# Kernel tuning notes

Measured on AMD Instinct MI355X. Metric: run time of the kernel, lower is better.

## Reference

```python
import jax, jax.numpy as jnp
import numpy as np

B, F, NUM_LAYERS, T, DEPTH, C = 256, 128, 4, 2048, 6, 100
L = 2 ** DEPTH  # num_leaves = 64

# bit pattern of the oblivious tree: bit d of leaf_idx (MSB-first),
# matching (leaf_idx // (L >> (d+1))) % 2 in the original double loop
_BITS = np.stack([(np.arange(L) // (L >> (d + 1))) % 2 for d in range(DEPTH)])  # [DEPTH, L]


def setup_inputs() -> dict:
    key = jax.random.key(0)
    k = jax.random.split(key, 5)
    x = jax.random.normal(k[0], (B, F), dtype=jnp.float32)
    sel_W = jax.random.normal(k[1], (NUM_LAYERS, T * DEPTH, F), dtype=jnp.float32) * 0.05
    sel_b = jax.random.normal(k[2], (NUM_LAYERS, T * DEPTH), dtype=jnp.float32) * 0.01
    out_W = jax.random.normal(k[3], (C, NUM_LAYERS * T * L), dtype=jnp.float32) * 0.002
    out_b = jax.random.normal(k[4], (C,), dtype=jnp.float32) * 0.01
    return {"x": x, "sel_W": sel_W, "sel_b": sel_b, "out_W": out_W, "out_b": out_b}


def reference(x, sel_W, sel_b, out_W, out_b):
    bits = jnp.asarray(_BITS, dtype=x.dtype)  # [DEPTH, L]
    layer_outputs = []
    for i in range(NUM_LAYERS):
        # feature selector linear -> [B, T, DEPTH] threshold responses
        fv = jax.nn.sigmoid(x @ sel_W[i].T + sel_b[i]).reshape(B, T, DEPTH)
        # leaf probability = prod over depth of (left or right prob per bit)
        leaf = jnp.ones((B, T, L), dtype=x.dtype)
        for d in range(DEPTH):  # fixed small structural loop (depth=6)
            p = fv[:, :, d:d + 1]                     # [B, T, 1] left prob
            bit = bits[d]                             # [L]
            leaf = leaf * (p * (1.0 - bit) + (1.0 - p) * bit)
        layer_outputs.append(leaf.reshape(B, T * L))
    combined = jnp.concatenate(layer_outputs, axis=1)  # [B, NUM_LAYERS*T*L]
    return combined @ out_W.T + out_b
```

## Files before the change

kernel.cpp:

```cpp
#include <hip/hip_runtime.h>

#define BB 256
#define FF 128
#define CC 100
#define KG 512
#define ITPB 16

typedef short bf16x8 __attribute__((ext_vector_type(8)));
typedef float f32x4 __attribute__((ext_vector_type(4)));
typedef _Float16 f16x8 __attribute__((ext_vector_type(8)));

#define LDS_BARRIER() asm volatile("s_waitcnt lgkmcnt(0)\n\ts_barrier" ::: "memory")

static __device__ inline unsigned short f2bf(float f) {
    unsigned u = __float_as_uint(f);
    u += 0x7fffu + ((u >> 16) & 1u);
    return (unsigned short)(u >> 16);
}
static __device__ inline float bf2f(unsigned short h) {
    return __uint_as_float(((unsigned)h) << 16);
}

__global__ __launch_bounds__(256) void fv_kernel(
    const float* __restrict__ x, const float* __restrict__ selW,
    const float* __restrict__ selb, unsigned short* __restrict__ fvout)
{
    __shared__ unsigned short wt[128 * 136];
    __shared__ unsigned short xt[128 * 136];
    __shared__ float sb[128];

    const int tid = threadIdx.x;
    const int m0 = blockIdx.x * 128;
    const int n0 = blockIdx.y * 128;

    #pragma unroll 4
    for (int pass = 0; pass < 16; ++pass) {
        int idx = pass * 256 + tid;
        int r = idx >> 5, f4 = idx & 31;
        float4 v = *((const float4*)(selW + (size_t)(m0 + r) * FF) + f4);
        float4 vx = *((const float4*)(x + (size_t)(n0 + r) * FF) + f4);
        ushort4 h;
        h.x = f2bf(v.x); h.y = f2bf(v.y); h.z = f2bf(v.z); h.w = f2bf(v.w);
        *(ushort4*)(wt + r * 136 + f4 * 4) = h;
        ushort4 hx;
        hx.x = f2bf(vx.x); hx.y = f2bf(vx.y); hx.z = f2bf(vx.z); hx.w = f2bf(vx.w);
        *(ushort4*)(xt + r * 136 + f4 * 4) = hx;
    }
    if (tid < 128) sb[tid] = selb[m0 + tid];
    __syncthreads();

    const int w = tid >> 6, lane = tid & 63;
    const int q = lane >> 4, l15 = lane & 15;
    const int mq = w & 1, nq = w >> 1;

    f32x4 zero4 = {0.f, 0.f, 0.f, 0.f};
    f32x4 acc[4][4];
    #pragma unroll
    for (int i = 0; i < 4; ++i)
        #pragma unroll
        for (int j = 0; j < 4; ++j) acc[i][j] = zero4;

    #pragma unroll
    for (int ch = 0; ch < 4; ++ch) {
        bf16x8 a[4];
        #pragma unroll
        for (int ms = 0; ms < 4; ++ms)
            a[ms] = *(const bf16x8*)(wt + (mq * 64 + ms * 16 + l15) * 136 + ch * 32 + q * 8);
        #pragma unroll
        for (int ns = 0; ns < 4; ++ns) {
            bf16x8 bfr = *(const bf16x8*)(xt + (nq * 64 + ns * 16 + l15) * 136 + ch * 32 + q * 8);
            #pragma unroll
            for (int ms = 0; ms < 4; ++ms)
                acc[ms][ns] = __builtin_amdgcn_mfma_f32_16x16x32_bf16(a[ms], bfr, acc[ms][ns], 0, 0, 0);
        }
    }

    #pragma unroll
    for (int ms = 0; ms < 4; ++ms) {
        int rowl = mq * 64 + ms * 16 + q * 4;
        #pragma unroll
        for (int ns = 0; ns < 4; ++ns) {
            int b = n0 + nq * 64 + ns * 16 + l15;
            #pragma unroll
            for (int reg = 0; reg < 4; ++reg) {
                int row = m0 + rowl + reg;
                float z = acc[ms][ns][reg] + sb[rowl + reg];
                float p = 1.0f / (1.0f + __expf(-z));
                fvout[(size_t)row * 256 + b] = f2bf(p);
            }
        }
    }
}

__global__ __launch_bounds__(256, 2) void main_gemm(
    const unsigned short* __restrict__ fv, const float* __restrict__ outW,
    _Float16* __restrict__ part16)
{
    __shared__ unsigned short leaf[256 * 72];
    __shared__ unsigned short wt[112 * 72];

    const int tid = threadIdx.x;
    const int kg = blockIdx.x;
    const int w = tid >> 6, lane = tid & 63;
    const int q = lane >> 4, l15 = lane & 15;
    const int cc = tid >> 4, f4 = tid & 15;

    f32x4 zero4 = {0.f, 0.f, 0.f, 0.f};
    f32x4 acc[4][7];
    #pragma unroll
    for (int i = 0; i < 4; ++i)
        #pragma unroll
        for (int j = 0; j < 7; ++j) acc[i][j] = zero4;

    float4 wv[2][7];
    unsigned short pv[2][6];
    #pragma unroll
    for (int pb = 0; pb < 2; ++pb) {
        const int it = kg * ITPB + pb;
        #pragma unroll
        for (int pass = 0; pass < 7; ++pass) {
            const int c = pass * 16 + cc;
            float4 v = make_float4(0.f, 0.f, 0.f, 0.f);
            if (c < CC)
                v = *((const float4*)(outW + (size_t)c * 524288 + (size_t)it * 64) + f4);
            wv[pb][pass] = v;
        }
        const unsigned short* fp = fv + (size_t)it * 1536 + tid;
        #pragma unroll
        for (int d = 0; d < 6; ++d) pv[pb][d] = fp[d * 256];
    }

    #pragma unroll 2
    for (int itl = 0; itl < ITPB; ++itl) {
        const int cur = itl & 1;
        LDS_BARRIER();

        #pragma unroll
        for (int pass = 0; pass < 7; ++pass) {
            const int c = pass * 16 + cc;
            ushort4 h;
            h.x = f2bf(wv[cur][pass].x); h.y = f2bf(wv[cur][pass].y);
            h.z = f2bf(wv[cur][pass].z); h.w = f2bf(wv[cur][pass].w);
            *(ushort4*)(wt + c * 72 + f4 * 4) = h;
        }

        {
            float p0 = bf2f(pv[cur][0]), p1 = bf2f(pv[cur][1]), p2 = bf2f(pv[cur][2]);
            float p3 = bf2f(pv[cur][3]), p4 = bf2f(pv[cur][4]), p5 = bf2f(pv[cur][5]);
            float q0 = 1.f - p0, q1 = 1.f - p1, q2 = 1.f - p2;
            float q3 = 1.f - p3, q4 = 1.f - p4, q5 = 1.f - p5;
            float A[4]  = {p0 * p1, p0 * q1, q0 * p1, q0 * q1};
            float B2[4] = {p2 * p3, p2 * q3, q2 * p3, q2 * q3};
            float C2[4] = {p4 * p5, p4 * q5, q4 * p5, q4 * q5};
            float BC[16];
            #pragma unroll
            for (int m = 0; m < 16; ++m) BC[m] = B2[m >> 2] * C2[m & 3];
            unsigned short* row = leaf + tid * 72;
            #pragma unroll
            for (int j = 0; j < 8; ++j) {
                uint4 dw;
                unsigned int* dwp = (unsigned int*)&dw;
                #pragma unroll
                for (int e = 0; e < 4; ++e) {
                    int l0 = j * 8 + 2 * e;
                    float v0 = A[l0 >> 4] * BC[l0 & 15];
                    float v1 = A[(l0 + 1) >> 4] * BC[(l0 + 1) & 15];
                    dwp[e] = (unsigned)f2bf(v0) | ((unsigned)f2bf(v1) << 16);
                }
                *(uint4*)(row + j * 8) = dw;
            }
        }

        {
            const int itn = kg * ITPB + ((itl + 2) & (ITPB - 1));
            #pragma unroll
            for (int pass = 0; pass < 7; ++pass) {
                const int c = pass * 16 + cc;
                if (c < CC)
                    wv[cur][pass] = *((const float4*)(outW + (size_t)c * 524288 + (size_t)itn * 64) + f4);
            }
            const unsigned short* fp = fv + (size_t)itn * 1536 + tid;
            #pragma unroll
            for (int d = 0; d < 6; ++d) pv[cur][d] = fp[d * 256];
        }

        LDS_BARRIER();

        #pragma unroll
        for (int ch = 0; ch < 2; ++ch) {
            bf16x8 a[4];
            #pragma unroll
            for (int ms = 0; ms < 4; ++ms)
                a[ms] = *(const bf16x8*)(leaf + (w * 64 + ms * 16 + l15) * 72 + ch * 32 + q * 8);
            #pragma unroll
            for (int nt = 0; nt < 7; ++nt) {
                bf16x8 bb = *(const bf16x8*)(wt + (nt * 16 + l15) * 72 + ch * 32 + q * 8);
                #pragma unroll
                for (int ms = 0; ms < 4; ++ms)
                    acc[ms][nt] = __builtin_amdgcn_mfma_f32_16x16x32_bf16(a[ms], bb, acc[ms][nt], 0, 0, 0);
            }
        }
    }

    #pragma unroll
    for (int ms = 0; ms < 4; ++ms) {
        const int brow = w * 64 + ms * 16 + q * 4;
        #pragma unroll
        for (int nt = 0; nt < 7; ++nt) {
            const int c = nt * 16 + l15;
            #pragma unroll
            for (int reg = 0; reg < 4; ++reg)
                part16[((size_t)(brow + reg) * KG + kg) * 112 + c] =
                    (_Float16)acc[ms][nt][reg];
        }
    }
}

__global__ __launch_bounds__(256) void reduce_k(
    const _Float16* __restrict__ part16, const float* __restrict__ outb,
    float* __restrict__ out)
{
    __shared__ float red[16 * 112];
    const int b = blockIdx.x;
    const int tid = threadIdx.x;
    const f16x8* slice = (const f16x8*)(part16 + (size_t)b * (KG * 112));

    if (tid < 224) {
        const int c8 = tid % 14;
        const int kgs = tid / 14;
        float s[8];
        #pragma unroll
        for (int j = 0; j < 8; ++j) s[j] = 0.f;
        #pragma unroll 4
        for (int i = 0; i < 32; ++i) {
            f16x8 v = slice[i * 224 + tid];
            #pragma unroll
            for (int j = 0; j < 8; ++j) s[j] += (float)v[j];
        }
        #pragma unroll
        for (int j = 0; j < 8; ++j) red[kgs * 112 + c8 * 8 + j] = s[j];
    }
    __syncthreads();
    if (tid < CC) {
        float r = outb[tid];
        #pragma unroll
        for (int k = 0; k < 16; ++k) r += red[k * 112 + tid];
        out[b * CC + tid] = r;
    }
}

extern "C" void kernel_launch(void* const* d_in, const int* in_sizes, int n_in,
                              void* d_out, int out_size, void* d_ws, size_t ws_size,
                              hipStream_t stream) {
    const float* x    = (const float*)d_in[0];
    const float* selW = (const float*)d_in[1];
    const float* selb = (const float*)d_in[2];
    const float* outW = (const float*)d_in[3];
    const float* outb = (const float*)d_in[4];
    float* out = (float*)d_out;

    unsigned short* fv = (unsigned short*)d_ws;
    _Float16* part16 = (_Float16*)((char*)d_ws + 25165824);

    fv_kernel<<<dim3(384, 2), 256, 0, stream>>>(x, selW, selb, fv);
    main_gemm<<<KG, 256, 0, stream>>>(fv, outW, part16);
    reduce_k<<<BB, 256, 0, stream>>>(part16, outb, out);
}
```

Baseline: 374.9 us.

## Stage out_W via global_load_lds and double the K-split of main GEMM

Loads the fp32 out_W tile directly from global memory into LDS with global_load_lds, then converts it to bf16 B fragments when reading from LDS. This replaces the register prefetch plus the separate bf16 store into a transposed LDS tile. KG doubles to 1024 with half as many iterations per block, which spreads the work over more blocks, and the reduce kernel's loop grows to match. The old two-deep register double-buffer becomes a single stage with a vmcnt(0) wait each iteration. That can expose load latency, and the larger KG doubles the partial-sum traffic the reduce kernel has to read.

```diff
diff --git a/kernel.cpp b/kernel.cpp
--- a/kernel.cpp
+++ b/kernel.cpp
@@ -1,16 +1,18 @@
 #include <hip/hip_runtime.h>
+#include <hip/hip_bf16.h>
 
 #define BB 256
 #define FF 128
 #define CC 100
-#define KG 512
-#define ITPB 16
+#define KG 1024
+#define ITPB 8
 
 typedef short bf16x8 __attribute__((ext_vector_type(8)));
 typedef float f32x4 __attribute__((ext_vector_type(4)));
 typedef _Float16 f16x8 __attribute__((ext_vector_type(8)));
 
 #define LDS_BARRIER() asm volatile("s_waitcnt lgkmcnt(0)\n\ts_barrier" ::: "memory")
+#define WAIT_VM0() asm volatile("s_waitcnt vmcnt(0)" ::: "memory")
 
 static __device__ inline unsigned short f2bf(float f) {
     unsigned u = __float_as_uint(f);
@@ -19,6 +21,16 @@
 }
 static __device__ inline float bf2f(unsigned short h) {
     return __uint_as_float(((unsigned)h) << 16);
+}
+static __device__ inline unsigned pk2(float a, float b) {
+    __hip_bfloat162 h = __float22bfloat162_rn(float2{a, b});
+    union { __hip_bfloat162 h2; unsigned u; } cv; cv.h2 = h;
+    return cv.u;
+}
+static __device__ inline void gl_lds16(const float* g, float* l) {
+    __builtin_amdgcn_global_load_lds(
+        (const __attribute__((address_space(1))) void*)g,
+        (__attribute__((address_space(3))) void*)l, 16, 0, 0);
 }
 
 __global__ __launch_bounds__(256) void fv_kernel(
@@ -96,14 +108,13 @@
     const unsigned short* __restrict__ fv, const float* __restrict__ outW,
     _Float16* __restrict__ part16)
 {
+    __shared__ float stage[7168];
     __shared__ unsigned short leaf[256 * 72];
-    __shared__ unsigned short wt[112 * 72];
 
     const int tid = threadIdx.x;
     const int kg = blockIdx.x;
     const int w = tid >> 6, lane = tid & 63;
     const int q = lane >> 4, l15 = lane & 15;
-    const int cc = tid >> 4, f4 = tid & 15;
 
     f32x4 zero4 = {0.f, 0.f, 0.f, 0.f};
     f32x4 acc[4][7];
@@ -112,41 +123,31 @@
         #pragma unroll
         for (int j = 0; j < 7; ++j) acc[i][j] = zero4;
 
-    float4 wv[2][7];
-    unsigned short pv[2][6];
-    #pragma unroll
-    for (int pb = 0; pb < 2; ++pb) {
-        const int it = kg * ITPB + pb;
-        #pragma unroll
-        for (int pass = 0; pass < 7; ++pass) {
-            const int c = pass * 16 + cc;
-            float4 v = make_float4(0.f, 0.f, 0.f, 0.f);
-            if (c < CC)
-                v = *((const float4*)(outW + (size_t)c * 524288 + (size_t)it * 64) + f4);
-            wv[pb][pass] = v;
-        }
+    int kk4[7], ccl[7];
+    #pragma unroll
+    for (int j = 0; j < 7; ++j) {
+        unsigned s = (unsigned)(w * 7 + j) * 64u + (unsigned)lane;
+        unsigned k4 = s / 112u, c = s % 112u;
+        kk4[j] = (int)k4;
+        ccl[j] = (c < CC) ? (int)c : 0;
+    }
+
+    unsigned short pv[6];
+    {
+        const int it = kg * ITPB;
         const unsigned short* fp = fv + (size_t)it * 1536 + tid;
         #pragma unroll
-        for (int d = 0; d < 6; ++d) pv[pb][d] = fp[d * 256];
-    }
-
-    #pragma unroll 2
+        for (int d = 0; d < 6; ++d) pv[d] = fp[d * 256];
+        #pragma unroll
+        for (int j = 0; j < 7; ++j)
+            gl_lds16(outW + (size_t)ccl[j] * 524288 + (size_t)it * 64 + kk4[j] * 4,
+                     stage + (w * 7 + j) * 256);
+    }
+
     for (int itl = 0; itl < ITPB; ++itl) {
-        const int cur = itl & 1;
-        LDS_BARRIER();
-
-        #pragma unroll
-        for (int pass = 0; pass < 7; ++pass) {
-            const int c = pass * 16 + cc;
-            ushort4 h;
-            h.x = f2bf(wv[cur][pass].x); h.y = f2bf(wv[cur][pass].y);
-            h.z = f2bf(wv[cur][pass].z); h.w = f2bf(wv[cur][pass].w);
-            *(ushort4*)(wt + c * 72 + f4 * 4) = h;
-        }
-
         {
-            float p0 = bf2f(pv[cur][0]), p1 = bf2f(pv[cur][1]), p2 = bf2f(pv[cur][2]);
-            float p3 = bf2f(pv[cur][3]), p4 = bf2f(pv[cur][4]), p5 = bf2f(pv[cur][5]);
+            float p0 = bf2f(pv[0]), p1 = bf2f(pv[1]), p2 = bf2f(pv[2]);
+            float p3 = bf2f(pv[3]), p4 = bf2f(pv[4]), p5 = bf2f(pv[5]);
             float q0 = 1.f - p0, q1 = 1.f - p1, q2 = 1.f - p2;
             float q3 = 1.f - p3, q4 = 1.f - p4, q5 = 1.f - p5;
             float A[4]  = {p0 * p1, p0 * q1, q0 * p1, q0 * q1};
@@ -163,42 +164,55 @@
                 #pragma unroll
                 for (int e = 0; e < 4; ++e) {
                     int l0 = j * 8 + 2 * e;
-                    float v0 = A[l0 >> 4] * BC[l0 & 15];
-                    float v1 = A[(l0 + 1) >> 4] * BC[(l0 + 1) & 15];
-                    dwp[e] = (unsigned)f2bf(v0) | ((unsigned)f2bf(v1) << 16);
+                    dwp[e] = (unsigned)f2bf(A[l0 >> 4] * BC[l0 & 15]) |
+                             ((unsigned)f2bf(A[(l0 + 1) >> 4] * BC[(l0 + 1) & 15]) << 16);
                 }
                 *(uint4*)(row + j * 8) = dw;
             }
         }
 
-        {
-            const int itn = kg * ITPB + ((itl + 2) & (ITPB - 1));
-            #pragma unroll
-            for (int pass = 0; pass < 7; ++pass) {
-                const int c = pass * 16 + cc;
-                if (c < CC)
-                    wv[cur][pass] = *((const float4*)(outW + (size_t)c * 524288 + (size_t)itn * 64) + f4);
+        WAIT_VM0();
+        LDS_BARRIER();
+
+        #pragma unroll
+        for (int ch = 0; ch < 2; ++ch) {
+            const int k4a = ch * 8 + q * 2;
+            bf16x8 bfrag[7];
+            #pragma unroll
+            for (int nt = 0; nt < 7; ++nt) {
+                const int c = nt * 16 + l15;
+                const float* sp = stage + (size_t)(k4a * 112 + c) * 4;
+                f32x4 lo = *(const f32x4*)sp;
+                f32x4 hi = *(const f32x4*)(sp + 448);
+                union { bf16x8 v; unsigned u[4]; } bu;
+                bu.u[0] = pk2(lo[0], lo[1]);
+                bu.u[1] = pk2(lo[2], lo[3]);
+                bu.u[2] = pk2(hi[0], hi[1]);
+                bu.u[3] = pk2(hi[2], hi[3]);
+                bfrag[nt] = bu.v;
             }
-            const unsigned short* fp = fv + (size_t)itn * 1536 + tid;
-            #pragma unroll
-            for (int d = 0; d < 6; ++d) pv[cur][d] = fp[d * 256];
-        }
-
-        LDS_BARRIER();
-
-        #pragma unroll
-        for (int ch = 0; ch < 2; ++ch) {
             bf16x8 a[4];
             #pragma unroll
             for (int ms = 0; ms < 4; ++ms)
                 a[ms] = *(const bf16x8*)(leaf + (w * 64 + ms * 16 + l15) * 72 + ch * 32 + q * 8);
             #pragma unroll
-            for (int nt = 0; nt < 7; ++nt) {
-                bf16x8 bb = *(const bf16x8*)(wt + (nt * 16 + l15) * 72 + ch * 32 + q * 8);
+            for (int nt = 0; nt < 7; ++nt)
                 #pragma unroll
                 for (int ms = 0; ms < 4; ++ms)
-                    acc[ms][nt] = __builtin_amdgcn_mfma_f32_16x16x32_bf16(a[ms], bb, acc[ms][nt], 0, 0, 0);
-            }
+                    acc[ms][nt] = __builtin_amdgcn_mfma_f32_16x16x32_bf16(a[ms], bfrag[nt], acc[ms][nt], 0, 0, 0);
+        }
+
+        LDS_BARRIER();
+
+        if (itl + 1 < ITPB) {
+            const int itn = kg * ITPB + itl + 1;
+            const unsigned short* fp = fv + (size_t)itn * 1536 + tid;
+            #pragma unroll
+            for (int d = 0; d < 6; ++d) pv[d] = fp[d * 256];
+            #pragma unroll
+            for (int j = 0; j < 7; ++j)
+                gl_lds16(outW + (size_t)ccl[j] * 524288 + (size_t)itn * 64 + kk4[j] * 4,
+                         stage + (w * 7 + j) * 256);
         }
     }
 
@@ -232,7 +246,7 @@
         #pragma unroll
         for (int j = 0; j < 8; ++j) s[j] = 0.f;
         #pragma unroll 4
-        for (int i = 0; i < 32; ++i) {
+        for (int i = 0; i < 64; ++i) {
             f16x8 v = slice[i * 224 + tid];
             #pragma unroll
             for (int j = 0; j < 8; ++j) s[j] += (float)v[j];
```

After: 399.8 us. +6.6%, slower.

## Pre-pack out_W into MFMA fragment layout and build leaf fragments in registers

Applied to the files above, without the earlier changes.

Adds a separate kernel that converts out_W to bf16 and stores it in an MFMA-fragment-ordered layout in workspace. main_gemm then loads B fragments straight from global memory instead of staging through LDS. Leaf probabilities are no longer written to LDS; each wave broadcasts the fv values with shuffles and builds its A fragments in registers, which removes both LDS barriers. The cost is an extra pass that reads all of out_W and writes a bf16 copy each call, and main_gemm loses the two-iteration global prefetch of the weights.

```diff
diff --git a/kernel.cpp b/kernel.cpp
--- a/kernel.cpp
+++ b/kernel.cpp
@@ -1,16 +1,17 @@
 #include <hip/hip_runtime.h>
+#include <hip/hip_bf16.h>
 
 #define BB 256
 #define FF 128
 #define CC 100
 #define KG 512
 #define ITPB 16
+#define NIT 8192
+#define WT_IT 7168
 
 typedef short bf16x8 __attribute__((ext_vector_type(8)));
 typedef float f32x4 __attribute__((ext_vector_type(4)));
 typedef _Float16 f16x8 __attribute__((ext_vector_type(8)));
-
-#define LDS_BARRIER() asm volatile("s_waitcnt lgkmcnt(0)\n\ts_barrier" ::: "memory")
 
 static __device__ inline unsigned short f2bf(float f) {
     unsigned u = __float_as_uint(f);
@@ -19,6 +20,11 @@
 }
 static __device__ inline float bf2f(unsigned short h) {
     return __uint_as_float(((unsigned)h) << 16);
+}
+static __device__ inline unsigned pk2(float a, float b) {
+    __hip_bfloat162 h = __float22bfloat162_rn(float2{a, b});
+    union { __hip_bfloat162 h2; unsigned u; } cv; cv.h2 = h;
+    return cv.u;
 }
 
 __global__ __launch_bounds__(256) void fv_kernel(
@@ -92,18 +98,62 @@
     }
 }
 
+__global__ __launch_bounds__(256) void wt_kernel(
+    const float* __restrict__ outW, unsigned short* __restrict__ Wt)
+{
+    __shared__ unsigned short tile[WT_IT];
+    const int tid = threadIdx.x;
+    const int it = blockIdx.x;
+
+    #pragma unroll
+    for (int i = 0; i < 4; ++i) {
+        int s = i * 256 + tid;
+        if (s < 896) *(uint4*)(tile + s * 8) = make_uint4(0, 0, 0, 0);
+    }
+    __syncthreads();
+
+    const int cr = tid >> 4;
+    const int f4 = tid & 15;
+    const int ch4 = (f4 >> 3) * 4 + ((f4 >> 1) & 3);
+    const int j0 = (f4 & 1) * 4;
+
+    float4 v[7];
+    #pragma unroll
+    for (int pass = 0; pass < 7; ++pass) {
+        const int c = pass * 16 + cr;
+        v[pass] = make_float4(0.f, 0.f, 0.f, 0.f);
+        if (c < CC)
+            v[pass] = *((const float4*)(outW + (size_t)c * 524288 + (size_t)it * 64) + f4);
+    }
+    #pragma unroll
+    for (int pass = 0; pass < 7; ++pass) {
+        const int c = pass * 16 + cr;
+        if (c < CC) {
+            unsigned lo = pk2(v[pass].x, v[pass].y);
+            unsigned hi = pk2(v[pass].z, v[pass].w);
+            *(uint2*)(tile + (ch4 * 112 + c) * 8 + j0) = make_uint2(lo, hi);
+        }
+    }
+    __syncthreads();
+
+    uint4* dst = (uint4*)(Wt + (size_t)it * WT_IT);
+    const uint4* src = (const uint4*)tile;
+    #pragma unroll
+    for (int i = 0; i < 4; ++i) {
+        int s = i * 256 + tid;
+        if (s < 896) dst[s] = src[s];
+    }
+}
+
 __global__ __launch_bounds__(256, 2) void main_gemm(
-    const unsigned short* __restrict__ fv, const float* __restrict__ outW,
+    const unsigned short* __restrict__ fv, const unsigned short* __restrict__ Wt,
     _Float16* __restrict__ part16)
 {
-    __shared__ unsigned short leaf[256 * 72];
-    __shared__ unsigned short wt[112 * 72];
-
     const int tid = threadIdx.x;
     const int kg = blockIdx.x;
     const int w = tid >> 6, lane = tid & 63;
     const int q = lane >> 4, l15 = lane & 15;
-    const int cc = tid >> 4, f4 = tid & 15;
+    const int qh = q >> 1, ql = q & 1;
 
     f32x4 zero4 = {0.f, 0.f, 0.f, 0.f};
     f32x4 acc[4][7];
@@ -112,94 +162,74 @@
         #pragma unroll
         for (int j = 0; j < 7; ++j) acc[i][j] = zero4;
 
-    float4 wv[2][7];
-    unsigned short pv[2][6];
-    #pragma unroll
-    for (int pb = 0; pb < 2; ++pb) {
-        const int it = kg * ITPB + pb;
-        #pragma unroll
-        for (int pass = 0; pass < 7; ++pass) {
-            const int c = pass * 16 + cc;
-            float4 v = make_float4(0.f, 0.f, 0.f, 0.f);
-            if (c < CC)
-                v = *((const float4*)(outW + (size_t)c * 524288 + (size_t)it * 64) + f4);
-            wv[pb][pass] = v;
-        }
-        const unsigned short* fp = fv + (size_t)it * 1536 + tid;
-        #pragma unroll
-        for (int d = 0; d < 6; ++d) pv[pb][d] = fp[d * 256];
-    }
-
-    #pragma unroll 2
+    unsigned short pvb[2][6];
+    {
+        const unsigned short* fp = fv + (size_t)(kg * ITPB) * 1536 + tid;
+        #pragma unroll
+        for (int d = 0; d < 6; ++d) pvb[0][d] = fp[d * 256];
+    }
+
     for (int itl = 0; itl < ITPB; ++itl) {
+        const int it = kg * ITPB + itl;
         const int cur = itl & 1;
-        LDS_BARRIER();
-
-        #pragma unroll
-        for (int pass = 0; pass < 7; ++pass) {
-            const int c = pass * 16 + cc;
-            ushort4 h;
-            h.x = f2bf(wv[cur][pass].x); h.y = f2bf(wv[cur][pass].y);
-            h.z = f2bf(wv[cur][pass].z); h.w = f2bf(wv[cur][pass].w);
-            *(ushort4*)(wt + c * 72 + f4 * 4) = h;
-        }
-
-        {
-            float p0 = bf2f(pv[cur][0]), p1 = bf2f(pv[cur][1]), p2 = bf2f(pv[cur][2]);
-            float p3 = bf2f(pv[cur][3]), p4 = bf2f(pv[cur][4]), p5 = bf2f(pv[cur][5]);
-            float q0 = 1.f - p0, q1 = 1.f - p1, q2 = 1.f - p2;
-            float q3 = 1.f - p3, q4 = 1.f - p4, q5 = 1.f - p5;
-            float A[4]  = {p0 * p1, p0 * q1, q0 * p1, q0 * q1};
-            float B2[4] = {p2 * p3, p2 * q3, q2 * p3, q2 * q3};
-            float C2[4] = {p4 * p5, p4 * q5, q4 * p5, q4 * q5};
-            float BC[16];
-            #pragma unroll
-            for (int m = 0; m < 16; ++m) BC[m] = B2[m >> 2] * C2[m & 3];
-            unsigned short* row = leaf + tid * 72;
-            #pragma unroll
-            for (int j = 0; j < 8; ++j) {
-                uint4 dw;
-                unsigned int* dwp = (unsigned int*)&dw;
-                #pragma unroll
-                for (int e = 0; e < 4; ++e) {
-                    int l0 = j * 8 + 2 * e;
-                    float v0 = A[l0 >> 4] * BC[l0 & 15];
-                    float v1 = A[(l0 + 1) >> 4] * BC[(l0 + 1) & 15];
-                    dwp[e] = (unsigned)f2bf(v0) | ((unsigned)f2bf(v1) << 16);
-                }
-                *(uint4*)(row + j * 8) = dw;
+
+        if (itl + 1 < ITPB) {
+            const unsigned short* fp = fv + (size_t)(it + 1) * 1536 + tid;
+            #pragma unroll
+            for (int d = 0; d < 6; ++d) pvb[cur ^ 1][d] = fp[d * 256];
+        }
+
+        const unsigned short* wbase = Wt + (size_t)it * WT_IT;
+        bf16x8 bfr[2][7];
+        #pragma unroll
+        for (int ch = 0; ch < 2; ++ch)
+            #pragma unroll
+            for (int nt = 0; nt < 7; ++nt)
+                bfr[ch][nt] = *(const bf16x8*)(wbase + ((ch * 4 + q) * 112 + nt * 16 + l15) * 8);
+
+        float p[6];
+        #pragma unroll
+        for (int d = 0; d < 6; ++d) p[d] = bf2f(pvb[cur][d]);
+
+        bf16x8 afr[4][2];
+        #pragma unroll
+        for (int ms = 0; ms < 4; ++ms) {
+            const int src = ms * 16 + l15;
+            float s0 = __shfl(p[0], src, 64);
+            float s1 = __shfl(p[1], src, 64);
+            float s2 = __shfl(p[2], src, 64);
+            float s3 = __shfl(p[3], src, 64);
+            float s4 = __shfl(p[4], src, 64);
+            float s5 = __shfl(p[5], src, 64);
+            float t1 = qh ? (1.f - s1) : s1;
+            float A0 = s0 * t1;
+            float A1 = (1.f - s0) * t1;
+            float t2 = ql ? (1.f - s2) : s2;
+            float Bv0 = t2 * s3;
+            float Bv1 = t2 * (1.f - s3);
+            float n4 = 1.f - s4, n5 = 1.f - s5;
+            float Cv0 = s4 * s5, Cv1 = s4 * n5, Cv2 = n4 * s5, Cv3 = n4 * n5;
+            #pragma unroll
+            for (int ch = 0; ch < 2; ++ch) {
+                float A = ch ? A1 : A0;
+                float ab0 = A * Bv0, ab1 = A * Bv1;
+                union { bf16x8 v; unsigned u[4]; } bu;
+                bu.u[0] = pk2(ab0 * Cv0, ab0 * Cv1);
+                bu.u[1] = pk2(ab0 * Cv2, ab0 * Cv3);
+                bu.u[2] = pk2(ab1 * Cv0, ab1 * Cv1);
+                bu.u[3] = pk2(ab1 * Cv2, ab1 * Cv3);
+                afr[ms][ch] = bu.v;
             }
         }
 
-        {
-            const int itn = kg * ITPB + ((itl + 2) & (ITPB - 1));
-            #pragma unroll
-            for (int pass = 0; pass < 7; ++pass) {
-                const int c = pass * 16 + cc;
-                if (c < CC)
-                    wv[cur][pass] = *((const float4*)(outW + (size_t)c * 524288 + (size_t)itn * 64) + f4);
-            }
-            const unsigned short* fp = fv + (size_t)itn * 1536 + tid;
-            #pragma unroll
-            for (int d = 0; d < 6; ++d) pv[cur][d] = fp[d * 256];
-        }
-
-        LDS_BARRIER();
-
-        #pragma unroll
-        for (int ch = 0; ch < 2; ++ch) {
-            bf16x8 a[4];
-            #pragma unroll
-            for (int ms = 0; ms < 4; ++ms)
-                a[ms] = *(const bf16x8*)(leaf + (w * 64 + ms * 16 + l15) * 72 + ch * 32 + q * 8);
-            #pragma unroll
-            for (int nt = 0; nt < 7; ++nt) {
-                bf16x8 bb = *(const bf16x8*)(wt + (nt * 16 + l15) * 72 + ch * 32 + q * 8);
+        #pragma unroll
+        for (int ch = 0; ch < 2; ++ch)
+            #pragma unroll
+            for (int nt = 0; nt < 7; ++nt)
                 #pragma unroll
                 for (int ms = 0; ms < 4; ++ms)
-                    acc[ms][nt] = __builtin_amdgcn_mfma_f32_16x16x32_bf16(a[ms], bb, acc[ms][nt], 0, 0, 0);
-            }
-        }
+                    acc[ms][nt] = __builtin_amdgcn_mfma_f32_16x16x32_bf16(
+                        afr[ms][ch], bfr[ch][nt], acc[ms][nt], 0, 0, 0);
     }
 
     #pragma unroll
@@ -260,9 +290,11 @@
     float* out = (float*)d_out;
 
     unsigned short* fv = (unsigned short*)d_ws;
-    _Float16* part16 = (_Float16*)((char*)d_ws + 25165824);
-
+    unsigned short* Wt = (unsigned short*)((char*)d_ws + 25165824);
+    _Float16* part16 = (_Float16*)((char*)d_ws + 142606336);
+
+    wt_kernel<<<NIT, 256, 0, stream>>>(outW, Wt);
     fv_kernel<<<dim3(384, 2), 256, 0, stream>>>(x, selW, selb, fv);
-    main_gemm<<<KG, 256, 0, stream>>>(fv, outW, part16);
+    main_gemm<<<KG, 256, 0, stream>>>(fv, Wt, part16);
     reduce_k<<<BB, 256, 0, stream>>>(part16, outb, out);
 }
```

After: 421.3 us. 1.12x slower.
